# Kernel optimization log

Hardware: AMD Instinct MI355X
Metric: run time of the kernel (lower is better)

The kernel has to match this reference:

```python
import jax, jax.numpy as jnp
import numpy as np

T = 20000          # document length in tokens
EMBED_DIM = 300    # GloVe 840B.300d
STATE_DIM = 400    # 2 * lstm_dim (bidirectional)
HIDDEN = 150       # Scorer hidden_dim default
MAX_N = 10         # span widths 1..10
G_DIM = 2 * STATE_DIM + EMBED_DIM  # 1100


def _mlp3(x, W1, b1, W2, b2, W3, b3):
    # Scorer: Linear -> ReLU -> Linear -> ReLU -> Linear(->1)
    h = jax.nn.relu(x @ W1 + b1)
    h = jax.nn.relu(h @ W2 + b2)
    return h @ W3 + b3


def _span_features(embeds, states, attn_logits):
    """Vectorized SpanEncoder: for every window of width n in 1..MAX_N,
    softmax the per-token attention logits within the window, attention-pool
    the word embeddings, and concat [state_start, state_end, pooled].
    Returns g of shape [sum_n (T-n+1), G_DIM]."""
    gs = []
    for n in range(1, MAX_N + 1):
        S = T - n + 1  # number of width-n spans
        # [n, S] windowed logits and [n, S, E] windowed embeds via shifted slices
        a = jnp.stack([attn_logits[j:j + S] for j in range(n)], axis=0)
        w = jax.nn.softmax(a, axis=0)  # softmax within each span (dim=0 in torch)
        we = jnp.stack([embeds[j:j + S] for j in range(n)], axis=0)
        pooled = jnp.einsum('ns,nse->se', w, we)  # [S, E]
        g = jnp.concatenate([states[:S], states[n - 1:n - 1 + S], pooled], axis=-1)
        gs.append(g)
    return jnp.concatenate(gs, axis=0)


def setup_inputs() -> dict:
    key = jax.random.key(0)
    ks = jax.random.split(key, 16)
    sc = 0.05
    return {
        'embeds': jax.random.normal(ks[0], (T, EMBED_DIM), jnp.float32),
        'states': jax.random.normal(ks[1], (T, STATE_DIM), jnp.float32),
        'attn_W1': jax.random.normal(ks[2], (STATE_DIM, HIDDEN), jnp.float32) * sc,
        'attn_b1': jnp.zeros((HIDDEN,), jnp.float32),
        'attn_W2': jax.random.normal(ks[3], (HIDDEN, HIDDEN), jnp.float32) * sc,
        'attn_b2': jnp.zeros((HIDDEN,), jnp.float32),
        'attn_W3': jax.random.normal(ks[4], (HIDDEN, 1), jnp.float32) * sc,
        'attn_b3': jnp.zeros((1,), jnp.float32),
        'sc_W1': jax.random.normal(ks[5], (G_DIM, HIDDEN), jnp.float32) * sc,
        'sc_b1': jnp.zeros((HIDDEN,), jnp.float32),
        'sc_W2': jax.random.normal(ks[6], (HIDDEN, HIDDEN), jnp.float32) * sc,
        'sc_b2': jnp.zeros((HIDDEN,), jnp.float32),
        'sc_W3': jax.random.normal(ks[7], (HIDDEN, 1), jnp.float32) * sc,
        'sc_b3': jnp.zeros((1,), jnp.float32),
    }


def reference(embeds, states, attn_W1, attn_b1, attn_W2, attn_b2, attn_W3, attn_b3,
              sc_W1, sc_b1, sc_W2, sc_b2, sc_W3, sc_b3):
    # SpanAttention: per-token scalar attention logit from the BiLSTM state
    attn_logits = _mlp3(states, attn_W1, attn_b1, attn_W2, attn_b2, attn_W3, attn_b3)[:, 0]
    # SpanEncoder: ragged windowed attention pooling + boundary-state concat
    g = _span_features(embeds, states, attn_logits)  # [10T-45, 1100]
    # SpanScorer: MLP score per span
    scores = _mlp3(g, sc_W1, sc_b1, sc_W2, sc_b2, sc_W3, sc_b3)[:, 0]
    return scores
```

## Files before the change

### kernel.cpp

```cpp
#include <hip/hip_runtime.h>
#include <hip/hip_bf16.h>
#include <math.h>

#define T_LEN 20000
#define HID 150

typedef __attribute__((ext_vector_type(8))) __bf16 bf16x8;
typedef __attribute__((ext_vector_type(4))) float f32x4;

__device__ __forceinline__ short f2bf(float f) {
    unsigned u = __float_as_uint(f);
    u = (u + 0x7fff + ((u >> 16) & 1)) >> 16;
    return (short)u;
}

__device__ __forceinline__ unsigned pk2(float a, float b) {
    __hip_bfloat162 h = __float22bfloat162_rn(make_float2(a, b));
    return *(unsigned*)&h;
}

__device__ __forceinline__ bf16x8 cvt8(float4 a, float4 b) {
    union { unsigned u[4]; bf16x8 v; } r;
    r.u[0] = pk2(a.x, a.y);
    r.u[1] = pk2(a.z, a.w);
    r.u[2] = pk2(b.x, b.y);
    r.u[3] = pk2(b.z, b.w);
    return r.v;
}

__device__ __forceinline__ float2 ubf2(unsigned u) {
    return make_float2(__uint_as_float(u << 16),
                       __uint_as_float(u & 0xffff0000u));
}

__global__ __launch_bounds__(256) void wprep(
    const float* __restrict__ sc_W1, const float* __restrict__ attn_W1,
    const float* __restrict__ attn_W2, const float* __restrict__ sc_W2,
    short* __restrict__ frag)
{
    int t = blockIdx.x * 256 + threadIdx.x;
    if (t >= 302080) return;
    float v = 0.f;
    if (t < 199680) {
        int e = t & 7, g = t >> 3;
        int lane = g & 63, h = g >> 6;
        int ks = h % 13, nt = h / 13;
        int k = ks * 32 + (lane >> 4) * 8 + e;
        int cs = (nt % 10) * 16 + (lane & 15);
        if (k < 400 && cs < HID) {
            if (nt < 10)      v = sc_W1[(long)k * HID + cs];
            else if (nt < 20) v = sc_W1[(long)(400 + k) * HID + cs];
            else              v = attn_W1[(long)k * HID + cs];
        }
    } else if (t < 250880) {
        int r = t - 199680;
        int e = r & 7, g = r >> 3;
        int lane = g & 63, h = g >> 6;
        int ks = h % 10, nt = h / 10;
        int k = ks * 32 + (lane >> 4) * 8 + e;
        int cs = nt * 16 + (lane & 15);
        if (k < 300 && cs < HID) v = sc_W1[(long)(800 + k) * HID + cs];
    } else if (t < 276480) {
        int r = t - 250880;
        int e = r & 7, g = r >> 3;
        int lane = g & 63, h = g >> 6;
        int ks = h % 5, nt = h / 5;
        int k = ks * 32 + (lane >> 4) * 8 + e;
        int cs = nt * 16 + (lane & 15);
        if (k < HID && cs < HID) v = attn_W2[(long)k * HID + cs];
    } else {
        int r = t - 276480;
        int e = r & 7, g = r >> 3;
        int lane = g & 63, h = g >> 6;
        int ks = h % 5, nt = h / 5;
        int k = ks * 32 + (lane >> 4) * 8 + e;
        int cs = nt * 16 + (lane & 15);
        if (k < HID && cs < HID) v = sc_W2[(long)k * HID + cs];
    }
    frag[t] = f2bf(v);
}

__global__ __launch_bounds__(256) void fusedA(
    const float* __restrict__ states, const short* __restrict__ frag,
    const float* __restrict__ scb1, const float* __restrict__ ab1,
    const float* __restrict__ ab2, const float* __restrict__ aW3,
    const float* __restrict__ ab3,
    short* __restrict__ Ubf, short* __restrict__ Vbf, float* __restrict__ logits)
{
    __shared__ short h1s[16 * 168];
    __shared__ float red[16][4];
    __shared__ float sb1[160], ab1s[160];
    const int tid = threadIdx.x;
    const int w = tid >> 6, lane = tid & 63;
    const int ml = lane & 15, kg = lane >> 4;
    const int m0 = blockIdx.x * 16;

    for (int t = tid; t < 160; t += 256) {
        sb1[t]  = (t < HID) ? scb1[t] : 0.f;
        ab1s[t] = (t < HID) ? ab1[t]  : 0.f;
    }
    __syncthreads();

    const float* Arow = states + (long)(m0 + ml) * 400;
    const int nT = (w < 2) ? 8 : 7;

    f32x4 acc[8];
    #pragma unroll
    for (int t = 0; t < 8; ++t) acc[t] = (f32x4){0.f, 0.f, 0.f, 0.f};

    for (int ks = 0; ks < 13; ++ks) {
        int k = ks * 32 + kg * 8;
        float4 a0 = make_float4(0.f, 0.f, 0.f, 0.f);
        float4 a1 = make_float4(0.f, 0.f, 0.f, 0.f);
        if (k + 4 <= 400) a0 = *(const float4*)&Arow[k];
        if (k + 8 <= 400) a1 = *(const float4*)&Arow[k + 4];
        bf16x8 af = cvt8(a0, a1);
        #pragma unroll
        for (int t = 0; t < 8; ++t) {
            if (t < nT) {
                int nt = 4 * t + w;
                bf16x8 bf = *(const bf16x8*)&frag[(long)(((nt * 13 + ks) << 6) | lane) << 3];
                acc[t] = __builtin_amdgcn_mfma_f32_16x16x32_bf16(bf, af, acc[t], 0, 0, 0);
            }
        }
    }

    #pragma unroll
    for (int t = 0; t < 8; ++t) {
        if (t < nT) {
            int nt = 4 * t + w;
            if (nt < 10) {
                int col0 = nt * 16 + kg * 4;
                float v[4];
                #pragma unroll
                for (int r = 0; r < 4; ++r) {
                    int c = col0 + r;
                    v[r] = (c < HID) ? acc[t][r] + sb1[c] : 0.f;
                }
                *(uint2*)&Ubf[(long)(m0 + ml) * 160 + col0] =
                    make_uint2(pk2(v[0], v[1]), pk2(v[2], v[3]));
            } else if (nt < 20) {
                int col0 = (nt - 10) * 16 + kg * 4;
                float v[4];
                #pragma unroll
                for (int r = 0; r < 4; ++r) {
                    int c = col0 + r;
                    v[r] = (c < HID) ? acc[t][r] : 0.f;
                }
                *(uint2*)&Vbf[(long)(m0 + ml) * 160 + col0] =
                    make_uint2(pk2(v[0], v[1]), pk2(v[2], v[3]));
            } else {
                int col0 = (nt - 20) * 16 + kg * 4;
                float v[4];
                #pragma unroll
                for (int r = 0; r < 4; ++r) {
                    int c = col0 + r;
                    v[r] = (c < HID) ? fmaxf(acc[t][r] + ab1s[c], 0.f) : 0.f;
                }
                *(uint2*)&h1s[ml * 168 + col0] =
                    make_uint2(pk2(v[0], v[1]), pk2(v[2], v[3]));
            }
        }
    }
    __syncthreads();

    const short* fAt2 = frag + 250880;
    bf16x8 af2[5];
    #pragma unroll
    for (int ks = 0; ks < 5; ++ks)
        af2[ks] = *(const bf16x8*)&h1s[ml * 168 + ks * 32 + kg * 8];

    const int nT2 = (w < 2) ? 3 : 2;
    float score[4] = {0.f, 0.f, 0.f, 0.f};
    #pragma unroll
    for (int t = 0; t < 3; ++t) {
        if (t < nT2) {
            int nt = 4 * t + w;
            f32x4 a2 = {0.f, 0.f, 0.f, 0.f};
            #pragma unroll
            for (int ks = 0; ks < 5; ++ks) {
                bf16x8 bf = *(const bf16x8*)&fAt2[(long)(((nt * 5 + ks) << 6) | lane) << 3];
                a2 = __builtin_amdgcn_mfma_f32_16x16x32_bf16(af2[ks], bf, a2, 0, 0, 0);
            }
            int col = nt * 16 + ml;
            float b2v = (col < HID) ? ab2[col] : 0.f;
            float w3v = (col < HID) ? aW3[col] : 0.f;
            #pragma unroll
            for (int r = 0; r < 4; ++r)
                score[r] += fmaxf(a2[r] + b2v, 0.f) * w3v;
        }
    }
    #pragma unroll
    for (int r = 0; r < 4; ++r) {
        score[r] += __shfl_xor(score[r], 1);
        score[r] += __shfl_xor(score[r], 2);
        score[r] += __shfl_xor(score[r], 4);
        score[r] += __shfl_xor(score[r], 8);
    }
    if (ml == 0) {
        #pragma unroll
        for (int r = 0; r < 4; ++r) red[kg * 4 + r][w] = score[r];
    }
    __syncthreads();
    if (tid < 16)
        logits[m0 + tid] = red[tid][0] + red[tid][1] + red[tid][2] + red[tid][3] + ab3[0];
}

__global__ __launch_bounds__(256) void pkern(
    const float* __restrict__ embeds, const short* __restrict__ frag,
    short* __restrict__ Pbf)
{
    const int tid = threadIdx.x;
    const int w = tid >> 6, lane = tid & 63;
    const int ml = lane & 15, kg = lane >> 4;
    const int m0 = blockIdx.x * 16;
    const short* fP = frag + 199680;

    const float* Arow = embeds + (long)(m0 + ml) * 300;
    const int nT = (w < 2) ? 3 : 2;

    f32x4 acc[3];
    #pragma unroll
    for (int t = 0; t < 3; ++t) acc[t] = (f32x4){0.f, 0.f, 0.f, 0.f};

    for (int ks = 0; ks < 10; ++ks) {
        int k = ks * 32 + kg * 8;
        float4 a0 = make_float4(0.f, 0.f, 0.f, 0.f);
        float4 a1 = make_float4(0.f, 0.f, 0.f, 0.f);
        if (k + 4 <= 300) a0 = *(const float4*)&Arow[k];
        if (k + 8 <= 300) a1 = *(const float4*)&Arow[k + 4];
        bf16x8 af = cvt8(a0, a1);
        #pragma unroll
        for (int t = 0; t < 3; ++t) {
            if (t < nT) {
                int nt = 4 * t + w;
                bf16x8 bf = *(const bf16x8*)&fP[(long)(((nt * 10 + ks) << 6) | lane) << 3];
                acc[t] = __builtin_amdgcn_mfma_f32_16x16x32_bf16(bf, af, acc[t], 0, 0, 0);
            }
        }
    }

    #pragma unroll
    for (int t = 0; t < 3; ++t) {
        if (t < nT) {
            int nt = 4 * t + w;
            int col0 = nt * 16 + kg * 4;
            float v[4];
            #pragma unroll
            for (int r = 0; r < 4; ++r) {
                int c = col0 + r;
                v[r] = (c < HID) ? acc[t][r] : 0.f;
            }
            *(uint2*)&Pbf[(long)(m0 + ml) * 160 + col0] =
                make_uint2(pk2(v[0], v[1]), pk2(v[2], v[3]));
        }
    }
}

__global__ __launch_bounds__(256) void span_all(
    const short* __restrict__ Ubf, const short* __restrict__ Vbf,
    const short* __restrict__ Pbf, const float* __restrict__ logits,
    const short* __restrict__ fW2, const float* __restrict__ b2,
    const float* __restrict__ W3, const float* __restrict__ b3,
    float* __restrict__ out)
{
    __shared__ short h1s[32 * 168];
    __shared__ float Ls[48], ebuf[48];
    __shared__ float b2s[160], W3s[160];
    __shared__ float red[32][2];

    const int tid = threadIdx.x;
    const int s0 = blockIdx.x * 32;
    const int nlo = blockIdx.y ? 6 : 1;
    const int nhi = blockIdx.y ? 10 : 5;

    if (tid < 48) {
        int r = s0 + tid; if (r > T_LEN - 1) r = T_LEN - 1;
        Ls[tid] = (tid < 41) ? logits[r] : -1e30f;
    }
    for (int t = tid; t < 160; t += 256) {
        b2s[t] = (t < HID) ? b2[t] : 0.f;
        W3s[t] = (t < HID) ? W3[t] : 0.f;
    }
    __syncthreads();
    if (tid < 48) {
        float M = -1e30f;
        for (int t = 0; t < 41; ++t) M = fmaxf(M, Ls[t]);
        ebuf[tid] = (tid < 41) ? expf(Ls[tid] - M) : 0.f;
    }
    __syncthreads();

    const int i = tid >> 3;
    const int q = tid & 7;
    const int d0 = 20 * q;
    const int s = s0 + i;
    int su = s; if (su > T_LEN - 1) su = T_LEN - 1;

    float Ur[20];
    {
        const uint2* U2 = (const uint2*)&Ubf[(long)su * 160 + d0];
        #pragma unroll
        for (int c = 0; c < 5; ++c) {
            uint2 uv = U2[c];
            float2 a = ubf2(uv.x), b_ = ubf2(uv.y);
            Ur[4 * c + 0] = a.x;  Ur[4 * c + 1] = a.y;
            Ur[4 * c + 2] = b_.x; Ur[4 * c + 3] = b_.y;
        }
    }
    float accp[20];
    #pragma unroll
    for (int d = 0; d < 20; ++d) accp[d] = 0.f;
    float den = 0.f;

    for (int j = 0; j < nlo - 1; ++j) {
        int rr_ = s + j; if (rr_ > T_LEN - 1) rr_ = T_LEN - 1;
        float e = ebuf[i + j];
        den += e;
        const uint2* P2 = (const uint2*)&Pbf[(long)rr_ * 160 + d0];
        #pragma unroll
        for (int c = 0; c < 5; ++c) {
            uint2 pv = P2[c];
            float2 a = ubf2(pv.x), b_ = ubf2(pv.y);
            accp[4 * c + 0] += e * a.x;  accp[4 * c + 1] += e * a.y;
            accp[4 * c + 2] += e * b_.x; accp[4 * c + 3] += e * b_.y;
        }
    }

    const int w = tid >> 6, lane = tid & 63;
    const int ml = lane & 15, kg = lane >> 4;
    const int mt = w >> 1;
    const int nt0 = (w & 1) * 5;
    const float bb = b3[0];

    for (int n = nlo; n <= nhi; ++n) {
        int rr_ = s + n - 1; if (rr_ > T_LEN - 1) rr_ = T_LEN - 1;
        float e = ebuf[i + n - 1];
        den += e;
        {
            const uint2* P2 = (const uint2*)&Pbf[(long)rr_ * 160 + d0];
            #pragma unroll
            for (int c = 0; c < 5; ++c) {
                uint2 pv = P2[c];
                float2 a = ubf2(pv.x), b_ = ubf2(pv.y);
                accp[4 * c + 0] += e * a.x;  accp[4 * c + 1] += e * a.y;
                accp[4 * c + 2] += e * b_.x; accp[4 * c + 3] += e * b_.y;
            }
        }
        float invd = 1.f / den;
        {
            const uint2* V2 = (const uint2*)&Vbf[(long)rr_ * 160 + d0];
            #pragma unroll
            for (int c = 0; c < 5; ++c) {
                uint2 vv = V2[c];
                float2 a = ubf2(vv.x), b_ = ubf2(vv.y);
                float x0 = fmaxf(Ur[4 * c + 0] + a.x  + accp[4 * c + 0] * invd, 0.f);
                float x1 = fmaxf(Ur[4 * c + 1] + a.y  + accp[4 * c + 1] * invd, 0.f);
                float x2 = fmaxf(Ur[4 * c + 2] + b_.x + accp[4 * c + 2] * invd, 0.f);
                float x3 = fmaxf(Ur[4 * c + 3] + b_.y + accp[4 * c + 3] * invd, 0.f);
                *(uint2*)&h1s[i * 168 + d0 + 4 * c] =
                    make_uint2(pk2(x0, x1), pk2(x2, x3));
            }
        }
        __syncthreads();

        bf16x8 af[5];
        #pragma unroll
        for (int ks = 0; ks < 5; ++ks)
            af[ks] = *(const bf16x8*)&h1s[(mt * 16 + ml) * 168 + ks * 32 + kg * 8];

        float sc[4] = {0.f, 0.f, 0.f, 0.f};
        #pragma unroll
        for (int j = 0; j < 5; ++j) {
            int nt = nt0 + j;
            f32x4 a2 = {0.f, 0.f, 0.f, 0.f};
            #pragma unroll
            for (int ks = 0; ks < 5; ++ks) {
                bf16x8 bf = *(const bf16x8*)&fW2[(long)(((nt * 5 + ks) << 6) | lane) << 3];
                a2 = __builtin_amdgcn_mfma_f32_16x16x32_bf16(af[ks], bf, a2, 0, 0, 0);
            }
            int col = nt * 16 + ml;
            float b2v = b2s[col], w3v = W3s[col];
            #pragma unroll
            for (int r = 0; r < 4; ++r)
                sc[r] += fmaxf(a2[r] + b2v, 0.f) * w3v;
        }
        #pragma unroll
        for (int r = 0; r < 4; ++r) {
            sc[r] += __shfl_xor(sc[r], 1);
            sc[r] += __shfl_xor(sc[r], 2);
            sc[r] += __shfl_xor(sc[r], 4);
            sc[r] += __shfl_xor(sc[r], 8);
        }
        if (ml == 0) {
            #pragma unroll
            for (int r = 0; r < 4; ++r)
                red[mt * 16 + kg * 4 + r][w & 1] = sc[r];
        }
        __syncthreads();
        if (tid < 32) {
            int S = T_LEN - n + 1;
            int off = (n - 1) * (T_LEN + 1) - (n - 1) * n / 2;
            int sr = s0 + tid;
            if (sr < S) out[off + sr] = red[tid][0] + red[tid][1] + bb;
        }
        __syncthreads();
    }
}

extern "C" void kernel_launch(void* const* d_in, const int* in_sizes, int n_in,
                              void* d_out, int out_size, void* d_ws, size_t ws_size,
                              hipStream_t stream) {
    const float* embeds  = (const float*)d_in[0];
    const float* states  = (const float*)d_in[1];
    const float* attn_W1 = (const float*)d_in[2];
    const float* attn_b1 = (const float*)d_in[3];
    const float* attn_W2 = (const float*)d_in[4];
    const float* attn_b2 = (const float*)d_in[5];
    const float* attn_W3 = (const float*)d_in[6];
    const float* attn_b3 = (const float*)d_in[7];
    const float* sc_W1   = (const float*)d_in[8];
    const float* sc_b1   = (const float*)d_in[9];
    const float* sc_W2   = (const float*)d_in[10];
    const float* sc_b2   = (const float*)d_in[11];
    const float* sc_W3   = (const float*)d_in[12];
    const float* sc_b3   = (const float*)d_in[13];
    float* out = (float*)d_out;

    short* wsS = (short*)d_ws;
    short* Ubf = wsS;
    short* Vbf = wsS + 3200256;
    short* Pbf = wsS + 6400512;
    short* frag = wsS + 9600768;
    float* logits = (float*)(wsS + 9902848);

    wprep<<<1180, 256, 0, stream>>>(sc_W1, attn_W1, attn_W2, sc_W2, frag);
    fusedA<<<1250, 256, 0, stream>>>(states, frag, sc_b1, attn_b1,
                                     attn_b2, attn_W3, attn_b3,
                                     Ubf, Vbf, logits);
    pkern<<<1250, 256, 0, stream>>>(embeds, frag, Pbf);
    span_all<<<dim3(625, 2), 256, 0, stream>>>(Ubf, Vbf, Pbf, logits,
                                               frag + 276480, sc_b2, sc_W3, sc_b3,
                                               out);
}
```

Measured before the change: 200.0 us.

## Fuse embed projection into fusedA and double-buffer span_all phases

Merges the separate pkern embed projection into the fusedA kernel, removing one launch and letting the two GEMMs share a block. In span_all, the layer-1 build for the next span width is written into a second shared-memory buffer while the current width runs its MFMA layer-2 pass. This removes one barrier per iteration and overlaps the two phases. Also unrolls the states K-loop. The cost is more shared memory and registers per block, which can lower occupancy.

```diff
diff --git a/kernel.cpp b/kernel.cpp
--- a/kernel.cpp
+++ b/kernel.cpp
@@ -80,12 +80,14 @@
     frag[t] = f2bf(v);
 }
 
-__global__ __launch_bounds__(256) void fusedA(
-    const float* __restrict__ states, const short* __restrict__ frag,
+__global__ __launch_bounds__(256) void fusedAP(
+    const float* __restrict__ states, const float* __restrict__ embeds,
+    const short* __restrict__ frag,
     const float* __restrict__ scb1, const float* __restrict__ ab1,
     const float* __restrict__ ab2, const float* __restrict__ aW3,
     const float* __restrict__ ab3,
-    short* __restrict__ Ubf, short* __restrict__ Vbf, float* __restrict__ logits)
+    short* __restrict__ Ubf, short* __restrict__ Vbf, short* __restrict__ Pbf,
+    float* __restrict__ logits)
 {
     __shared__ short h1s[16 * 168];
     __shared__ float red[16][4];
@@ -108,6 +110,7 @@
     #pragma unroll
     for (int t = 0; t < 8; ++t) acc[t] = (f32x4){0.f, 0.f, 0.f, 0.f};
 
+    #pragma unroll
     for (int ks = 0; ks < 13; ++ks) {
         int k = ks * 32 + kg * 8;
         float4 a0 = make_float4(0.f, 0.f, 0.f, 0.f);
@@ -164,6 +167,49 @@
     }
     __syncthreads();
 
+    {
+        const short* fP = frag + 199680;
+        const float* Erow = embeds + (long)(m0 + ml) * 300;
+        const int nTp = (w < 2) ? 3 : 2;
+        f32x4 accP[3];
+        #pragma unroll
+        for (int t = 0; t < 3; ++t) accP[t] = (f32x4){0.f, 0.f, 0.f, 0.f};
+
+        #pragma unroll
+        for (int ks = 0; ks < 10; ++ks) {
+            int k = ks * 32 + kg * 8;
+            float4 a0 = make_float4(0.f, 0.f, 0.f, 0.f);
+            float4 a1 = make_float4(0.f, 0.f, 0.f, 0.f);
+            if (k + 4 <= 300) a0 = *(const float4*)&Erow[k];
+            if (k + 8 <= 300) a1 = *(const float4*)&Erow[k + 4];
+            bf16x8 af = cvt8(a0, a1);
+            #pragma unroll
+            for (int t = 0; t < 3; ++t) {
+                if (t < nTp) {
+                    int nt = 4 * t + w;
+                    bf16x8 bf = *(const bf16x8*)&fP[(long)(((nt * 10 + ks) << 6) | lane) << 3];
+                    accP[t] = __builtin_amdgcn_mfma_f32_16x16x32_bf16(bf, af, accP[t], 0, 0, 0);
+                }
+            }
+        }
+
+        #pragma unroll
+        for (int t = 0; t < 3; ++t) {
+            if (t < nTp) {
+                int nt = 4 * t + w;
+                int col0 = nt * 16 + kg * 4;
+                float v[4];
+                #pragma unroll
+                for (int r = 0; r < 4; ++r) {
+                    int c = col0 + r;
+                    v[r] = (c < HID) ? accP[t][r] : 0.f;
+                }
+                *(uint2*)&Pbf[(long)(m0 + ml) * 160 + col0] =
+                    make_uint2(pk2(v[0], v[1]), pk2(v[2], v[3]));
+            }
+        }
+    }
+
     const short* fAt2 = frag + 250880;
     bf16x8 af2[5];
     #pragma unroll
@@ -204,57 +250,6 @@
     __syncthreads();
     if (tid < 16)
         logits[m0 + tid] = red[tid][0] + red[tid][1] + red[tid][2] + red[tid][3] + ab3[0];
-}
-
-__global__ __launch_bounds__(256) void pkern(
-    const float* __restrict__ embeds, const short* __restrict__ frag,
-    short* __restrict__ Pbf)
-{
-    const int tid = threadIdx.x;
-    const int w = tid >> 6, lane = tid & 63;
-    const int ml = lane & 15, kg = lane >> 4;
-    const int m0 = blockIdx.x * 16;
-    const short* fP = frag + 199680;
-
-    const float* Arow = embeds + (long)(m0 + ml) * 300;
-    const int nT = (w < 2) ? 3 : 2;
-
-    f32x4 acc[3];
-    #pragma unroll
-    for (int t = 0; t < 3; ++t) acc[t] = (f32x4){0.f, 0.f, 0.f, 0.f};
-
-    for (int ks = 0; ks < 10; ++ks) {
-        int k = ks * 32 + kg * 8;
-        float4 a0 = make_float4(0.f, 0.f, 0.f, 0.f);
-        float4 a1 = make_float4(0.f, 0.f, 0.f, 0.f);
-        if (k + 4 <= 300) a0 = *(const float4*)&Arow[k];
-        if (k + 8 <= 300) a1 = *(const float4*)&Arow[k + 4];
-        bf16x8 af = cvt8(a0, a1);
-        #pragma unroll
-        for (int t = 0; t < 3; ++t) {
-            if (t < nT) {
-                int nt = 4 * t + w;
-                bf16x8 bf = *(const bf16x8*)&fP[(long)(((nt * 10 + ks) << 6) | lane) << 3];
-                acc[t] = __builtin_amdgcn_mfma_f32_16x16x32_bf16(bf, af, acc[t], 0, 0, 0);
-            }
-        }
-    }
-
-    #pragma unroll
-    for (int t = 0; t < 3; ++t) {
-        if (t < nT) {
-            int nt = 4 * t + w;
-            int col0 = nt * 16 + kg * 4;
-            float v[4];
-            #pragma unroll
-            for (int r = 0; r < 4; ++r) {
-                int c = col0 + r;
-                v[r] = (c < HID) ? acc[t][r] : 0.f;
-            }
-            *(uint2*)&Pbf[(long)(m0 + ml) * 160 + col0] =
-                make_uint2(pk2(v[0], v[1]), pk2(v[2], v[3]));
-        }
-    }
 }
 
 __global__ __launch_bounds__(256) void span_all(
@@ -264,10 +259,10 @@
     const float* __restrict__ W3, const float* __restrict__ b3,
     float* __restrict__ out)
 {
-    __shared__ short h1s[32 * 168];
+    __shared__ short h1s[2][32 * 168];
+    __shared__ float red[2][32][2];
     __shared__ float Ls[48], ebuf[48];
     __shared__ float b2s[160], W3s[160];
-    __shared__ float red[32][2];
 
     const int tid = threadIdx.x;
     const int s0 = blockIdx.x * 32;
@@ -332,7 +327,7 @@
     const int nt0 = (w & 1) * 5;
     const float bb = b3[0];
 
-    for (int n = nlo; n <= nhi; ++n) {
+    auto phase1 = [&](int n, int p) {
         int rr_ = s + n - 1; if (rr_ > T_LEN - 1) rr_ = T_LEN - 1;
         float e = ebuf[i + n - 1];
         den += e;
@@ -357,16 +352,23 @@
                 float x1 = fmaxf(Ur[4 * c + 1] + a.y  + accp[4 * c + 1] * invd, 0.f);
                 float x2 = fmaxf(Ur[4 * c + 2] + b_.x + accp[4 * c + 2] * invd, 0.f);
                 float x3 = fmaxf(Ur[4 * c + 3] + b_.y + accp[4 * c + 3] * invd, 0.f);
-                *(uint2*)&h1s[i * 168 + d0 + 4 * c] =
+                *(uint2*)&h1s[p][i * 168 + d0 + 4 * c] =
                     make_uint2(pk2(x0, x1), pk2(x2, x3));
             }
         }
-        __syncthreads();
+    };
+
+    phase1(nlo, 0);
+    __syncthreads();
+
+    for (int n = nlo; n <= nhi; ++n) {
+        const int p = (n - nlo) & 1;
+        if (n < nhi) phase1(n + 1, 1 - p);
 
         bf16x8 af[5];
         #pragma unroll
         for (int ks = 0; ks < 5; ++ks)
-            af[ks] = *(const bf16x8*)&h1s[(mt * 16 + ml) * 168 + ks * 32 + kg * 8];
+            af[ks] = *(const bf16x8*)&h1s[p][(mt * 16 + ml) * 168 + ks * 32 + kg * 8];
 
         float sc[4] = {0.f, 0.f, 0.f, 0.f};
         #pragma unroll
@@ -394,16 +396,15 @@
         if (ml == 0) {
             #pragma unroll
             for (int r = 0; r < 4; ++r)
-                red[mt * 16 + kg * 4 + r][w & 1] = sc[r];
+                red[p][mt * 16 + kg * 4 + r][w & 1] = sc[r];
         }
         __syncthreads();
         if (tid < 32) {
             int S = T_LEN - n + 1;
             int off = (n - 1) * (T_LEN + 1) - (n - 1) * n / 2;
             int sr = s0 + tid;
-            if (sr < S) out[off + sr] = red[tid][0] + red[tid][1] + bb;
-        }
-        __syncthreads();
+            if (sr < S) out[off + sr] = red[p][tid][0] + red[p][tid][1] + bb;
+        }
     }
 }
 
@@ -434,10 +435,9 @@
     float* logits = (float*)(wsS + 9902848);
 
     wprep<<<1180, 256, 0, stream>>>(sc_W1, attn_W1, attn_W2, sc_W2, frag);
-    fusedA<<<1250, 256, 0, stream>>>(states, frag, sc_b1, attn_b1,
-                                     attn_b2, attn_W3, attn_b3,
-                                     Ubf, Vbf, logits);
-    pkern<<<1250, 256, 0, stream>>>(embeds, frag, Pbf);
+    fusedAP<<<1250, 256, 0, stream>>>(states, embeds, frag, sc_b1, attn_b1,
+                                      attn_b2, attn_W3, attn_b3,
+                                      Ubf, Vbf, Pbf, logits);
     span_all<<<dim3(625, 2), 256, 0, stream>>>(Ubf, Vbf, Pbf, logits,
                                                frag + 276480, sc_b2, sc_W3, sc_b3,
                                                out);
```

Result: faster. 191.5 us (-4.3%).
